# Kernel tuning notes

Measured on AMD Instinct MI355X. Metric: run time of the kernel, lower is better.

The kernel has to match this reference:

```python
import jax, jax.numpy as jnp
import numpy as np

NUM_HEADS = 16
HEIGHT = 32
WIDTH = 32
FEATURES_DIM = HEIGHT * WIDTH  # 1024
EMBED_DIM = 1024


def setup_inputs() -> dict:
    key = jax.random.key(0)
    ks = jax.random.split(key, 9)
    s_in = 1.0 / np.sqrt(FEATURES_DIM)
    s_e = 1.0 / np.sqrt(EMBED_DIM)
    return {
        "x": jax.random.normal(ks[0], (16, 512, HEIGHT, WIDTH), dtype=jnp.float32),
        "Wq": jax.random.uniform(ks[1], (EMBED_DIM, FEATURES_DIM), jnp.float32, -s_in, s_in),
        "bq": jax.random.uniform(ks[2], (EMBED_DIM,), jnp.float32, -s_in, s_in),
        "Wk": jax.random.uniform(ks[3], (EMBED_DIM, FEATURES_DIM), jnp.float32, -s_in, s_in),
        "bk": jax.random.uniform(ks[4], (EMBED_DIM,), jnp.float32, -s_in, s_in),
        "Wv": jax.random.uniform(ks[5], (EMBED_DIM, FEATURES_DIM), jnp.float32, -s_in, s_in),
        "bv": jax.random.uniform(ks[6], (EMBED_DIM,), jnp.float32, -s_in, s_in),
        "Wo": jax.random.uniform(ks[7], (FEATURES_DIM, EMBED_DIM), jnp.float32, -s_e, s_e),
        "bo": jax.random.uniform(ks[8], (FEATURES_DIM,), jnp.float32, -s_e, s_e),
    }


def reference(x, Wq, bq, Wk, bk, Wv, bv, Wo, bo):
    B, C, H, W = x.shape
    nh = NUM_HEADS
    hd = EMBED_DIM // nh
    xf = x.reshape(B, C, H * W)  # [B, C, F] - channel tokens
    q = xf @ Wq.T + bq  # [B, C, E]
    k = xf @ Wk.T + bk
    v = xf @ Wv.T + bv
    q = q.reshape(B, C, nh, hd).transpose(0, 2, 1, 3)  # [B, nh, C, hd]
    k = k.reshape(B, C, nh, hd).transpose(0, 2, 1, 3)
    v = v.reshape(B, C, nh, hd).transpose(0, 2, 1, 3)
    scores = jnp.einsum("bhcd,bhkd->bhck", q, k) / jnp.sqrt(jnp.float32(hd))
    attn = jax.nn.softmax(scores, axis=-1)
    out = jnp.einsum("bhck,bhkd->bhcd", attn, v)  # [B, nh, C, hd]
    out = out.transpose(0, 2, 1, 3).reshape(B, C, EMBED_DIM)
    out = out @ Wo.T + bo  # [B, C, F]
    return out.reshape(B, C, H, W)
```

## Files before the change

### kernel.cpp

```cpp
#include <hip/hip_runtime.h>


typedef unsigned short u16;
typedef __attribute__((ext_vector_type(8))) short short8;
typedef __attribute__((ext_vector_type(4))) float f32x4;
typedef __attribute__((ext_vector_type(4))) unsigned short u16x4;

#define MFMA16(a, b, c) __builtin_amdgcn_mfma_f32_16x16x32_bf16(a, b, c, 0, 0, 0)

__device__ __forceinline__ u16 f2bf(float x) {
  unsigned u = __float_as_uint(x);
  u += 0x7FFFu + ((u >> 16) & 1u);
  return (u16)(u >> 16);
}

__device__ __forceinline__ void async16(const void* g, void* l) {
  __builtin_amdgcn_global_load_lds(
      (__attribute__((address_space(1))) unsigned int*)(g),
      (__attribute__((address_space(3))) unsigned int*)(l), 16, 0, 0);
}

__global__ __launch_bounds__(256) void cvt_all(
    const float* __restrict__ x, const float* __restrict__ wq,
    const float* __restrict__ wk, const float* __restrict__ wv,
    const float* __restrict__ wo, u16* __restrict__ dst) {
  int g = blockIdx.x * 256 + threadIdx.x;
  const float* s;
  int off;
  if (g < 2097152) {
    s = x; off = g;
  } else {
    int r = g - 2097152;
    int w = r >> 18;
    off = r & 262143;
    s = (w == 0) ? wq : (w == 1) ? wk : (w == 2) ? wv : wo;
  }
  f32x4 v = ((const f32x4*)s)[off];
  u16x4 o;
#pragma unroll
  for (int j = 0; j < 4; ++j) o[j] = f2bf(v[j]);
  ((u16x4*)dst)[g] = o;
}

template <int CB, bool ST>
__device__ __forceinline__ void tile256(const u16* lds, const u16* gA,
                                        const u16* gB, u16* stA, u16* stB,
                                        int kn, int arow, int brow, int sw0,
                                        int sw1, short8* a, short8* b,
                                        f32x4 acc[8][4]) {
  constexpr int NB = CB ^ 1;
  const u16* bp = lds + CB * 32768;
#pragma unroll
  for (int mf = 0; mf < 4; ++mf) {
    a[mf * 2 + 0] = *(const short8*)(bp + arow + mf * 1024 + sw0);
    a[mf * 2 + 1] = *(const short8*)(bp + arow + mf * 1024 + sw1);
  }
#pragma unroll
  for (int nf = 0; nf < 2; ++nf) {
    b[nf * 2 + 0] = *(const short8*)(bp + brow + nf * 1024 + sw0);
    b[nf * 2 + 1] = *(const short8*)(bp + brow + nf * 1024 + sw1);
  }
  if (ST) {
    async16(gA + 0 * 65536 + kn, stA + NB * 32768 + 0 * 4096);
    async16(gA + 2 * 65536 + kn, stA + NB * 32768 + 2 * 4096);
    async16(gB + 0 * 65536 + kn, stB + NB * 32768 + 0 * 4096);
    async16(gB + 1 * 65536 + kn, stB + NB * 32768 + 1 * 4096);
  }
  __builtin_amdgcn_s_barrier();
  asm volatile("s_waitcnt lgkmcnt(0)" ::: "memory");
  __builtin_amdgcn_sched_barrier(0);
  __builtin_amdgcn_s_setprio(1);
#pragma unroll
  for (int mf = 0; mf < 4; ++mf)
#pragma unroll
    for (int nf = 0; nf < 2; ++nf) {
      acc[mf][nf] = MFMA16(a[mf * 2 + 0], b[nf * 2 + 0], acc[mf][nf]);
      acc[mf][nf] = MFMA16(a[mf * 2 + 1], b[nf * 2 + 1], acc[mf][nf]);
    }
  __builtin_amdgcn_s_setprio(0);
  __builtin_amdgcn_s_barrier();
#pragma unroll
  for (int nf = 2; nf < 4; ++nf) {
    b[nf * 2 + 0] = *(const short8*)(bp + brow + nf * 1024 + sw0);
    b[nf * 2 + 1] = *(const short8*)(bp + brow + nf * 1024 + sw1);
  }
  if (ST) {
    async16(gB + 2 * 65536 + kn, stB + NB * 32768 + 2 * 4096);
    async16(gB + 3 * 65536 + kn, stB + NB * 32768 + 3 * 4096);
  }
  __builtin_amdgcn_s_barrier();
  asm volatile("s_waitcnt lgkmcnt(0)" ::: "memory");
  __builtin_amdgcn_sched_barrier(0);
  __builtin_amdgcn_s_setprio(1);
#pragma unroll
  for (int mf = 0; mf < 4; ++mf)
#pragma unroll
    for (int nf = 2; nf < 4; ++nf) {
      acc[mf][nf] = MFMA16(a[mf * 2 + 0], b[nf * 2 + 0], acc[mf][nf]);
      acc[mf][nf] = MFMA16(a[mf * 2 + 1], b[nf * 2 + 1], acc[mf][nf]);
    }
  __builtin_amdgcn_s_setprio(0);
  __builtin_amdgcn_s_barrier();
#pragma unroll
  for (int mf = 4; mf < 8; ++mf) {
    a[(mf - 4) * 2 + 0] = *(const short8*)(bp + arow + mf * 1024 + sw0);
    a[(mf - 4) * 2 + 1] = *(const short8*)(bp + arow + mf * 1024 + sw1);
  }
  if (ST) {
    async16(gA + 1 * 65536 + kn, stA + NB * 32768 + 1 * 4096);
    async16(gA + 3 * 65536 + kn, stA + NB * 32768 + 3 * 4096);
  }
  __builtin_amdgcn_s_barrier();
  asm volatile("s_waitcnt lgkmcnt(0)" ::: "memory");
  __builtin_amdgcn_sched_barrier(0);
  __builtin_amdgcn_s_setprio(1);
#pragma unroll
  for (int mf = 4; mf < 8; ++mf)
#pragma unroll
    for (int nf = 2; nf < 4; ++nf) {
      acc[mf][nf] = MFMA16(a[(mf - 4) * 2 + 0], b[nf * 2 + 0], acc[mf][nf]);
      acc[mf][nf] = MFMA16(a[(mf - 4) * 2 + 1], b[nf * 2 + 1], acc[mf][nf]);
    }
  __builtin_amdgcn_s_setprio(0);
  __builtin_amdgcn_s_barrier();
  __builtin_amdgcn_s_setprio(1);
#pragma unroll
  for (int mf = 4; mf < 8; ++mf)
#pragma unroll
    for (int nf = 0; nf < 2; ++nf) {
      acc[mf][nf] = MFMA16(a[(mf - 4) * 2 + 0], b[nf * 2 + 0], acc[mf][nf]);
      acc[mf][nf] = MFMA16(a[(mf - 4) * 2 + 1], b[nf * 2 + 1], acc[mf][nf]);
    }
  __builtin_amdgcn_s_setprio(0);
  asm volatile("s_waitcnt vmcnt(0)" ::: "memory");
  __builtin_amdgcn_s_barrier();
}

__device__ __forceinline__ void gemm256(const u16* __restrict__ A,
                                        const u16* __restrict__ W, int m0,
                                        int n0, u16* lds, f32x4 acc[8][4]) {
  const int t = threadIdx.x;
  const int wave = t >> 6, lane = t & 63, lr = lane & 15, lg = lane >> 4;
  const int wr = wave >> 2, wn = wave & 3;
  const int srow = t >> 3;
  const int scol = ((t & 7) ^ (srow & 7)) << 3;
  const u16* gA = A + (size_t)(m0 + srow) * 1024 + scol;
  const u16* gB = W + (size_t)(n0 + srow) * 1024 + scol;
  u16* stA = lds + wave * 512;
  u16* stB = lds + 16384 + wave * 512;
  const int arow = (wr * 128 + lr) * 64;
  const int brow = 16384 + (wn * 64 + lr) * 64;
  const int xk = lr & 7;
  const int sw0 = (lg ^ xk) << 3;
  const int sw1 = ((4 + lg) ^ xk) << 3;

#pragma unroll
  for (int j = 0; j < 4; ++j) {
    async16(gA + j * 65536, stA + j * 4096);
    async16(gB + j * 65536, stB + j * 4096);
  }
  asm volatile("s_waitcnt vmcnt(0)" ::: "memory");
  __builtin_amdgcn_s_barrier();

  short8 a[8], b[8];
#pragma unroll 1
  for (int it = 0; it < 7; ++it) {
    const int kt = it * 2;
    tile256<0, true>(lds, gA, gB, stA, stB, (kt + 1) * 64, arow, brow, sw0,
                     sw1, a, b, acc);
    tile256<1, true>(lds, gA, gB, stA, stB, (kt + 2) * 64, arow, brow, sw0,
                     sw1, a, b, acc);
  }
  tile256<0, true>(lds, gA, gB, stA, stB, 15 * 64, arow, brow, sw0, sw1, a, b,
                   acc);
  tile256<1, false>(lds, gA, gB, stA, stB, 0, arow, brow, sw0, sw1, a, b, acc);
}

__global__ __launch_bounds__(512, 2) void gemm_qkv(
    const u16* __restrict__ xb, const u16* __restrict__ w3,
    const float* __restrict__ bq, const float* __restrict__ bk,
    const float* __restrict__ bv, u16* __restrict__ qo, u16* __restrict__ ko,
    u16* __restrict__ vo) {
  __shared__ u16 lds[65536];
  const int id = blockIdx.x;
  const int lid = (id & 7) * 48 + (id >> 3);
  const int tm = lid / 12, tn = lid % 12;
  const int m0 = tm * 256, n0g = tn * 256;
  const int z = n0g >> 10, n0 = n0g & 1023;
  const float* bias = (z == 0) ? bq : (z == 1) ? bk : bv;
  u16* outp = (z == 0) ? qo : (z == 1) ? ko : vo;
  f32x4 acc[8][4];
#pragma unroll
  for (int i = 0; i < 8; ++i)
#pragma unroll
    for (int j = 0; j < 4; ++j) acc[i][j] = (f32x4){0.f, 0.f, 0.f, 0.f};
  gemm256(xb, w3, m0, n0g, lds, acc);

  const int t = threadIdx.x;
  const int wave = t >> 6, lane = t & 63, lr = lane & 15, lg = lane >> 4;
  const int wr = wave >> 2, wn = wave & 3;
  float bb[4];
#pragma unroll
  for (int nf = 0; nf < 4; ++nf) bb[nf] = bias[n0 + wn * 64 + nf * 16 + lr];
#pragma unroll
  for (int mf = 0; mf < 8; ++mf)
#pragma unroll
    for (int nf = 0; nf < 4; ++nf)
#pragma unroll
      for (int r = 0; r < 4; ++r) {
        int m = m0 + wr * 128 + mf * 16 + lg * 4 + r;
        int n = n0 + wn * 64 + nf * 16 + lr;
        float val = acc[mf][nf][r] + bb[nf];
        int b_ = m >> 9, c = m & 511, h = n >> 6, dd = n & 63;
        int idx = (z == 2) ? ((((b_ << 4) + h) << 15) + (dd << 9) + c)
                           : ((((b_ << 4) + h) << 15) + (c << 6) + dd);
        outp[idx] = f2bf(val);
      }
}

__global__ __launch_bounds__(512, 2) void gemm_oproj(const u16* __restrict__ ab,
                                                     const u16* __restrict__ wo,
                                                     const float* __restrict__ bo,
                                                     float* __restrict__ out) {
  __shared__ u16 lds[65536];
  const int id = blockIdx.x;
  const int lid = (id & 7) * 16 + (id >> 3);
  const int m0 = (lid >> 2) * 256, n0 = (lid & 3) * 256;
  f32x4 acc[8][4];
#pragma unroll
  for (int i = 0; i < 8; ++i)
#pragma unroll
    for (int j = 0; j < 4; ++j) acc[i][j] = (f32x4){0.f, 0.f, 0.f, 0.f};
  gemm256(ab, wo, m0, n0, lds, acc);

  const int t = threadIdx.x;
  const int wave = t >> 6, lane = t & 63, lr = lane & 15, lg = lane >> 4;
  const int wr = wave >> 2, wn = wave & 3;
  float bb[4];
#pragma unroll
  for (int nf = 0; nf < 4; ++nf) bb[nf] = bo[n0 + wn * 64 + nf * 16 + lr];
#pragma unroll
  for (int mf = 0; mf < 8; ++mf)
#pragma unroll
    for (int nf = 0; nf < 4; ++nf)
#pragma unroll
      for (int r = 0; r < 4; ++r) {
        int m = m0 + wr * 128 + mf * 16 + lg * 4 + r;
        int n = n0 + wn * 64 + nf * 16 + lr;
        out[m * 1024 + n] = acc[mf][nf][r] + bb[nf];
      }
}

__global__ __launch_bounds__(512, 2) void attn_kernel(
    const u16* __restrict__ qb, const u16* __restrict__ kb,
    const u16* __restrict__ vb, u16* __restrict__ ab) {
  __shared__ u16 lK[32768];
  __shared__ u16 lV[32768];
  __shared__ u16 lP[8192];
  const int t = threadIdx.x;
  const int bh = blockIdx.x;
  const int b_ = bh >> 4, h_ = bh & 15;
  const u16* kg = kb + bh * 32768;
  const u16* vg = vb + bh * 32768;
#pragma unroll
  for (int i = 0; i < 8; ++i) {
    int row = i * 64 + (t >> 3), slot = t & 7;
    short8 kv = *(const short8*)(kg + row * 64 + slot * 8);
    *(short8*)(lK + row * 64 + ((slot ^ (row & 7)) << 3)) = kv;
    int vrow = i * 8 + (t >> 6), vslot = t & 63;
    short8 vv = *(const short8*)(vg + vrow * 512 + vslot * 8);
    *(short8*)(lV + vrow * 512 + ((vslot ^ (vrow & 7)) << 3)) = vv;
  }
  __syncthreads();

  const int wv_ = t >> 6, lane = t & 63, lr = lane & 15, lg = lane >> 4;
  u16* lPw = lP + wv_ * 1024;
  const u16* qg = qb + bh * 32768;
  const float sc = 0.125f * 1.44269504088896f;

#pragma unroll 1
  for (int qi = 0; qi < 4; ++qi) {
    const int qrow = (wv_ * 4 + qi) * 16;
    short8 a0 = *(const short8*)(qg + (qrow + lr) * 64 + lg * 8);
    short8 a1 = *(const short8*)(qg + (qrow + lr) * 64 + 32 + lg * 8);
    f32x4 s[32];
#pragma unroll
    for (int f = 0; f < 32; ++f) {
      const u16* kr = lK + (f * 16 + lr) * 64;
      short8 k0 = *(const short8*)(kr + ((lg ^ (lr & 7)) << 3));
      short8 k1 = *(const short8*)(kr + (((4 + lg) ^ (lr & 7)) << 3));
      f32x4 z4 = (f32x4){0.f, 0.f, 0.f, 0.f};
      z4 = MFMA16(a0, k0, z4);
      z4 = MFMA16(a1, k1, z4);
      s[f] = z4;
    }
    float inv[4];
#pragma unroll
    for (int r = 0; r < 4; ++r) {
      float m_ = s[0][r];
#pragma unroll
      for (int f = 1; f < 32; ++f) m_ = fmaxf(m_, s[f][r]);
      m_ = fmaxf(m_, __shfl_xor(m_, 1));
      m_ = fmaxf(m_, __shfl_xor(m_, 2));
      m_ = fmaxf(m_, __shfl_xor(m_, 4));
      m_ = fmaxf(m_, __shfl_xor(m_, 8));
      float sm = 0.f;
#pragma unroll
      for (int f = 0; f < 32; ++f) {
        float e = exp2f((s[f][r] - m_) * sc);
        s[f][r] = e;
        sm += e;
      }
      sm += __shfl_xor(sm, 1);
      sm += __shfl_xor(sm, 2);
      sm += __shfl_xor(sm, 4);
      sm += __shfl_xor(sm, 8);
      inv[r] = 1.f / sm;
    }
    f32x4 o[4];
#pragma unroll
    for (int i = 0; i < 4; ++i) o[i] = (f32x4){0.f, 0.f, 0.f, 0.f};
#pragma unroll
    for (int ch = 0; ch < 8; ++ch) {
#pragma unroll
      for (int cf = 0; cf < 4; ++cf)
#pragma unroll
        for (int r = 0; r < 4; ++r) {
          int q = lg * 4 + r, kc = cf * 16 + lr;
          lPw[q * 64 + (((kc >> 3) ^ (q & 7)) << 3) + (kc & 7)] =
              f2bf(s[ch * 4 + cf][r]);
        }
      asm volatile("s_waitcnt lgkmcnt(0)" ::: "memory");
      const u16* pr = lPw + lr * 64;
      short8 pa0 = *(const short8*)(pr + ((lg ^ (lr & 7)) << 3));
      short8 pa1 = *(const short8*)(pr + (((4 + lg) ^ (lr & 7)) << 3));
#pragma unroll
      for (int df = 0; df < 4; ++df) {
        const u16* vr = lV + (df * 16 + lr) * 512;
        short8 v0 = *(const short8*)(vr + (((ch * 8 + lg) ^ (lr & 7)) << 3));
        short8 v1 =
            *(const short8*)(vr + (((ch * 8 + 4 + lg) ^ (lr & 7)) << 3));
        o[df] = MFMA16(pa0, v0, o[df]);
        o[df] = MFMA16(pa1, v1, o[df]);
      }
    }
#pragma unroll
    for (int df = 0; df < 4; ++df)
#pragma unroll
      for (int r = 0; r < 4; ++r) {
        int q = qrow + lg * 4 + r, dd = df * 16 + lr;
        ab[(b_ * 512 + q) * 1024 + h_ * 64 + dd] = f2bf(o[df][r] * inv[r]);
      }
  }
}

extern "C" void kernel_launch(void* const* d_in, const int* in_sizes, int n_in,
                              void* d_out, int out_size, void* d_ws,
                              size_t ws_size, hipStream_t stream) {
  (void)in_sizes; (void)n_in; (void)out_size;
  const float* x  = (const float*)d_in[0];
  const float* Wq = (const float*)d_in[1];
  const float* bq = (const float*)d_in[2];
  const float* Wk = (const float*)d_in[3];
  const float* bk = (const float*)d_in[4];
  const float* Wv = (const float*)d_in[5];
  const float* bv = (const float*)d_in[6];
  const float* Wo = (const float*)d_in[7];
  const float* bo = (const float*)d_in[8];
  float* out = (float*)d_out;

  if (ws_size < 75497472u) return;
  u16* xb  = (u16*)d_ws;
  u16* w3b = xb + 8388608;
  u16* wob = w3b + 3145728;
  u16* qbuf = wob + 1048576;
  u16* kbuf = qbuf + 8388608;
  u16* vbuf = kbuf + 8388608;
  u16* abuf = xb;

  cvt_all<<<12288, 256, 0, stream>>>(x, Wq, Wk, Wv, Wo, xb);
  gemm_qkv<<<384, 512, 0, stream>>>(xb, w3b, bq, bk, bv, qbuf, kbuf, vbuf);
  attn_kernel<<<256, 512, 0, stream>>>(qbuf, kbuf, vbuf, abuf);
  gemm_oproj<<<128, 512, 0, stream>>>(abuf, wob, bo, out);
}
```

Measured before the change: 173.4 us.

## Deepen GEMM global-to-LDS prefetch pipeline and prefetch Q in attention

Restructures the GEMM main loop so each K tile's global-to-LDS async loads are split into halves issued one and two tiles ahead. Waits use a partial vmcnt instead of draining every outstanding load each tile. This is meant to hide more global memory latency behind MFMA work, at the cost of more LDS buffer hazards to get right. The attention kernel also loads all Q fragments into registers before the K/V staging barrier and raises wave priority around its MFMA blocks.

```diff
diff --git a/kernel.cpp b/kernel.cpp
--- a/kernel.cpp
+++ b/kernel.cpp
@@ -42,103 +42,9 @@
   ((u16x4*)dst)[g] = o;
 }
 
-template <int CB, bool ST>
-__device__ __forceinline__ void tile256(const u16* lds, const u16* gA,
-                                        const u16* gB, u16* stA, u16* stB,
-                                        int kn, int arow, int brow, int sw0,
-                                        int sw1, short8* a, short8* b,
-                                        f32x4 acc[8][4]) {
-  constexpr int NB = CB ^ 1;
-  const u16* bp = lds + CB * 32768;
-#pragma unroll
-  for (int mf = 0; mf < 4; ++mf) {
-    a[mf * 2 + 0] = *(const short8*)(bp + arow + mf * 1024 + sw0);
-    a[mf * 2 + 1] = *(const short8*)(bp + arow + mf * 1024 + sw1);
-  }
-#pragma unroll
-  for (int nf = 0; nf < 2; ++nf) {
-    b[nf * 2 + 0] = *(const short8*)(bp + brow + nf * 1024 + sw0);
-    b[nf * 2 + 1] = *(const short8*)(bp + brow + nf * 1024 + sw1);
-  }
-  if (ST) {
-    async16(gA + 0 * 65536 + kn, stA + NB * 32768 + 0 * 4096);
-    async16(gA + 2 * 65536 + kn, stA + NB * 32768 + 2 * 4096);
-    async16(gB + 0 * 65536 + kn, stB + NB * 32768 + 0 * 4096);
-    async16(gB + 1 * 65536 + kn, stB + NB * 32768 + 1 * 4096);
-  }
-  __builtin_amdgcn_s_barrier();
-  asm volatile("s_waitcnt lgkmcnt(0)" ::: "memory");
-  __builtin_amdgcn_sched_barrier(0);
-  __builtin_amdgcn_s_setprio(1);
-#pragma unroll
-  for (int mf = 0; mf < 4; ++mf)
-#pragma unroll
-    for (int nf = 0; nf < 2; ++nf) {
-      acc[mf][nf] = MFMA16(a[mf * 2 + 0], b[nf * 2 + 0], acc[mf][nf]);
-      acc[mf][nf] = MFMA16(a[mf * 2 + 1], b[nf * 2 + 1], acc[mf][nf]);
-    }
-  __builtin_amdgcn_s_setprio(0);
-  __builtin_amdgcn_s_barrier();
-#pragma unroll
-  for (int nf = 2; nf < 4; ++nf) {
-    b[nf * 2 + 0] = *(const short8*)(bp + brow + nf * 1024 + sw0);
-    b[nf * 2 + 1] = *(const short8*)(bp + brow + nf * 1024 + sw1);
-  }
-  if (ST) {
-    async16(gB + 2 * 65536 + kn, stB + NB * 32768 + 2 * 4096);
-    async16(gB + 3 * 65536 + kn, stB + NB * 32768 + 3 * 4096);
-  }
-  __builtin_amdgcn_s_barrier();
-  asm volatile("s_waitcnt lgkmcnt(0)" ::: "memory");
-  __builtin_amdgcn_sched_barrier(0);
-  __builtin_amdgcn_s_setprio(1);
-#pragma unroll
-  for (int mf = 0; mf < 4; ++mf)
-#pragma unroll
-    for (int nf = 2; nf < 4; ++nf) {
-      acc[mf][nf] = MFMA16(a[mf * 2 + 0], b[nf * 2 + 0], acc[mf][nf]);
-      acc[mf][nf] = MFMA16(a[mf * 2 + 1], b[nf * 2 + 1], acc[mf][nf]);
-    }
-  __builtin_amdgcn_s_setprio(0);
-  __builtin_amdgcn_s_barrier();
-#pragma unroll
-  for (int mf = 4; mf < 8; ++mf) {
-    a[(mf - 4) * 2 + 0] = *(const short8*)(bp + arow + mf * 1024 + sw0);
-    a[(mf - 4) * 2 + 1] = *(const short8*)(bp + arow + mf * 1024 + sw1);
-  }
-  if (ST) {
-    async16(gA + 1 * 65536 + kn, stA + NB * 32768 + 1 * 4096);
-    async16(gA + 3 * 65536 + kn, stA + NB * 32768 + 3 * 4096);
-  }
-  __builtin_amdgcn_s_barrier();
-  asm volatile("s_waitcnt lgkmcnt(0)" ::: "memory");
-  __builtin_amdgcn_sched_barrier(0);
-  __builtin_amdgcn_s_setprio(1);
-#pragma unroll
-  for (int mf = 4; mf < 8; ++mf)
-#pragma unroll
-    for (int nf = 2; nf < 4; ++nf) {
-      acc[mf][nf] = MFMA16(a[(mf - 4) * 2 + 0], b[nf * 2 + 0], acc[mf][nf]);
-      acc[mf][nf] = MFMA16(a[(mf - 4) * 2 + 1], b[nf * 2 + 1], acc[mf][nf]);
-    }
-  __builtin_amdgcn_s_setprio(0);
-  __builtin_amdgcn_s_barrier();
-  __builtin_amdgcn_s_setprio(1);
-#pragma unroll
-  for (int mf = 4; mf < 8; ++mf)
-#pragma unroll
-    for (int nf = 0; nf < 2; ++nf) {
-      acc[mf][nf] = MFMA16(a[(mf - 4) * 2 + 0], b[nf * 2 + 0], acc[mf][nf]);
-      acc[mf][nf] = MFMA16(a[(mf - 4) * 2 + 1], b[nf * 2 + 1], acc[mf][nf]);
-    }
-  __builtin_amdgcn_s_setprio(0);
-  asm volatile("s_waitcnt vmcnt(0)" ::: "memory");
-  __builtin_amdgcn_s_barrier();
-}
-
-__device__ __forceinline__ void gemm256(const u16* __restrict__ A,
-                                        const u16* __restrict__ W, int m0,
-                                        int n0, u16* lds, f32x4 acc[8][4]) {
+__device__ __forceinline__ void gemm8p(const u16* __restrict__ A,
+                                       const u16* __restrict__ W, int m0,
+                                       int n0, u16* lds, f32x4 acc[8][4]) {
   const int t = threadIdx.x;
   const int wave = t >> 6, lane = t & 63, lr = lane & 15, lg = lane >> 4;
   const int wr = wave >> 2, wn = wave & 3;
@@ -154,26 +60,111 @@
   const int sw0 = (lg ^ xk) << 3;
   const int sw1 = ((4 + lg) ^ xk) << 3;
 
-#pragma unroll
-  for (int j = 0; j < 4; ++j) {
-    async16(gA + j * 65536, stA + j * 4096);
-    async16(gB + j * 65536, stB + j * 4096);
-  }
-  asm volatile("s_waitcnt vmcnt(0)" ::: "memory");
+#define SA(kt, h)                                                           \
+  {                                                                         \
+    async16(gA + (2 * (h)) * 65536 + (kt) * 64,                             \
+            stA + ((kt) & 1) * 32768 + (2 * (h)) * 4096);                   \
+    async16(gA + (2 * (h) + 1) * 65536 + (kt) * 64,                         \
+            stA + ((kt) & 1) * 32768 + (2 * (h) + 1) * 4096);               \
+  }
+#define SB(kt, h)                                                           \
+  {                                                                         \
+    async16(gB + (2 * (h)) * 65536 + (kt) * 64,                             \
+            stB + ((kt) & 1) * 32768 + (2 * (h)) * 4096);                   \
+    async16(gB + (2 * (h) + 1) * 65536 + (kt) * 64,                         \
+            stB + ((kt) & 1) * 32768 + (2 * (h) + 1) * 4096);               \
+  }
+
+  SB(0, 0); SA(0, 0); SB(0, 1); SA(0, 1);
+  SB(1, 0); SA(1, 0);
+  asm volatile("s_waitcnt vmcnt(4)" ::: "memory");
   __builtin_amdgcn_s_barrier();
 
   short8 a[8], b[8];
-#pragma unroll 1
-  for (int it = 0; it < 7; ++it) {
-    const int kt = it * 2;
-    tile256<0, true>(lds, gA, gB, stA, stB, (kt + 1) * 64, arow, brow, sw0,
-                     sw1, a, b, acc);
-    tile256<1, true>(lds, gA, gB, stA, stB, (kt + 2) * 64, arow, brow, sw0,
-                     sw1, a, b, acc);
-  }
-  tile256<0, true>(lds, gA, gB, stA, stB, 15 * 64, arow, brow, sw0, sw1, a, b,
-                   acc);
-  tile256<1, false>(lds, gA, gB, stA, stB, 0, arow, brow, sw0, sw1, a, b, acc);
+#pragma unroll 2
+  for (int tt = 0; tt < 16; ++tt) {
+    const u16* bp = lds + (tt & 1) * 32768;
+#pragma unroll
+    for (int mf = 0; mf < 4; ++mf) {
+      a[mf * 2 + 0] = *(const short8*)(bp + arow + mf * 1024 + sw0);
+      a[mf * 2 + 1] = *(const short8*)(bp + arow + mf * 1024 + sw1);
+    }
+#pragma unroll
+    for (int nf = 0; nf < 2; ++nf) {
+      b[nf * 2 + 0] = *(const short8*)(bp + brow + nf * 1024 + sw0);
+      b[nf * 2 + 1] = *(const short8*)(bp + brow + nf * 1024 + sw1);
+    }
+    if (tt + 1 < 16) SB(tt + 1, 1);
+    __builtin_amdgcn_s_barrier();
+    asm volatile("s_waitcnt lgkmcnt(0)" ::: "memory");
+    __builtin_amdgcn_sched_barrier(0);
+    __builtin_amdgcn_s_setprio(1);
+#pragma unroll
+    for (int mf = 0; mf < 4; ++mf)
+#pragma unroll
+      for (int nf = 0; nf < 2; ++nf) {
+        acc[mf][nf] = MFMA16(a[mf * 2 + 0], b[nf * 2 + 0], acc[mf][nf]);
+        acc[mf][nf] = MFMA16(a[mf * 2 + 1], b[nf * 2 + 1], acc[mf][nf]);
+      }
+    __builtin_amdgcn_s_setprio(0);
+    __builtin_amdgcn_s_barrier();
+#pragma unroll
+    for (int nf = 2; nf < 4; ++nf) {
+      b[nf * 2 + 0] = *(const short8*)(bp + brow + nf * 1024 + sw0);
+      b[nf * 2 + 1] = *(const short8*)(bp + brow + nf * 1024 + sw1);
+    }
+    if (tt + 1 < 16) SA(tt + 1, 1);
+    __builtin_amdgcn_s_barrier();
+    asm volatile("s_waitcnt lgkmcnt(0)" ::: "memory");
+    __builtin_amdgcn_sched_barrier(0);
+    __builtin_amdgcn_s_setprio(1);
+#pragma unroll
+    for (int mf = 0; mf < 4; ++mf)
+#pragma unroll
+      for (int nf = 2; nf < 4; ++nf) {
+        acc[mf][nf] = MFMA16(a[mf * 2 + 0], b[nf * 2 + 0], acc[mf][nf]);
+        acc[mf][nf] = MFMA16(a[mf * 2 + 1], b[nf * 2 + 1], acc[mf][nf]);
+      }
+    __builtin_amdgcn_s_setprio(0);
+    __builtin_amdgcn_s_barrier();
+#pragma unroll
+    for (int mf = 4; mf < 8; ++mf) {
+      a[(mf - 4) * 2 + 0] = *(const short8*)(bp + arow + mf * 1024 + sw0);
+      a[(mf - 4) * 2 + 1] = *(const short8*)(bp + arow + mf * 1024 + sw1);
+    }
+    if (tt + 2 < 16) SB(tt + 2, 0);
+    __builtin_amdgcn_s_barrier();
+    asm volatile("s_waitcnt lgkmcnt(0)" ::: "memory");
+    __builtin_amdgcn_sched_barrier(0);
+    __builtin_amdgcn_s_setprio(1);
+#pragma unroll
+    for (int mf = 4; mf < 8; ++mf)
+#pragma unroll
+      for (int nf = 2; nf < 4; ++nf) {
+        acc[mf][nf] = MFMA16(a[(mf - 4) * 2 + 0], b[nf * 2 + 0], acc[mf][nf]);
+        acc[mf][nf] = MFMA16(a[(mf - 4) * 2 + 1], b[nf * 2 + 1], acc[mf][nf]);
+      }
+    __builtin_amdgcn_s_setprio(0);
+    __builtin_amdgcn_s_barrier();
+    if (tt + 2 < 16) SA(tt + 2, 0);
+    __builtin_amdgcn_s_setprio(1);
+#pragma unroll
+    for (int mf = 4; mf < 8; ++mf)
+#pragma unroll
+      for (int nf = 0; nf < 2; ++nf) {
+        acc[mf][nf] = MFMA16(a[(mf - 4) * 2 + 0], b[nf * 2 + 0], acc[mf][nf]);
+        acc[mf][nf] = MFMA16(a[(mf - 4) * 2 + 1], b[nf * 2 + 1], acc[mf][nf]);
+      }
+    __builtin_amdgcn_s_setprio(0);
+    if (tt < 14) {
+      asm volatile("s_waitcnt vmcnt(4)" ::: "memory");
+    } else {
+      asm volatile("s_waitcnt vmcnt(0)" ::: "memory");
+    }
+    __builtin_amdgcn_s_barrier();
+  }
+#undef SA
+#undef SB
 }
 
 __global__ __launch_bounds__(512, 2) void gemm_qkv(
@@ -194,7 +185,7 @@
   for (int i = 0; i < 8; ++i)
 #pragma unroll
     for (int j = 0; j < 4; ++j) acc[i][j] = (f32x4){0.f, 0.f, 0.f, 0.f};
-  gemm256(xb, w3, m0, n0g, lds, acc);
+  gemm8p(xb, w3, m0, n0g, lds, acc);
 
   const int t = threadIdx.x;
   const int wave = t >> 6, lane = t & 63, lr = lane & 15, lg = lane >> 4;
@@ -231,7 +222,7 @@
   for (int i = 0; i < 8; ++i)
 #pragma unroll
     for (int j = 0; j < 4; ++j) acc[i][j] = (f32x4){0.f, 0.f, 0.f, 0.f};
-  gemm256(ab, wo, m0, n0, lds, acc);
+  gemm8p(ab, wo, m0, n0, lds, acc);
 
   const int t = threadIdx.x;
   const int wave = t >> 6, lane = t & 63, lr = lane & 15, lg = lane >> 4;
@@ -271,29 +262,37 @@
     short8 vv = *(const short8*)(vg + vrow * 512 + vslot * 8);
     *(short8*)(lV + vrow * 512 + ((vslot ^ (vrow & 7)) << 3)) = vv;
   }
-  __syncthreads();
 
   const int wv_ = t >> 6, lane = t & 63, lr = lane & 15, lg = lane >> 4;
   u16* lPw = lP + wv_ * 1024;
   const u16* qg = qb + bh * 32768;
   const float sc = 0.125f * 1.44269504088896f;
 
+  short8 a0q[4], a1q[4];
+#pragma unroll
+  for (int qi = 0; qi < 4; ++qi) {
+    const int qrow = (wv_ * 4 + qi) * 16;
+    a0q[qi] = *(const short8*)(qg + (qrow + lr) * 64 + lg * 8);
+    a1q[qi] = *(const short8*)(qg + (qrow + lr) * 64 + 32 + lg * 8);
+  }
+  __syncthreads();
+
 #pragma unroll 1
   for (int qi = 0; qi < 4; ++qi) {
     const int qrow = (wv_ * 4 + qi) * 16;
-    short8 a0 = *(const short8*)(qg + (qrow + lr) * 64 + lg * 8);
-    short8 a1 = *(const short8*)(qg + (qrow + lr) * 64 + 32 + lg * 8);
     f32x4 s[32];
+    __builtin_amdgcn_s_setprio(1);
 #pragma unroll
     for (int f = 0; f < 32; ++f) {
       const u16* kr = lK + (f * 16 + lr) * 64;
       short8 k0 = *(const short8*)(kr + ((lg ^ (lr & 7)) << 3));
       short8 k1 = *(const short8*)(kr + (((4 + lg) ^ (lr & 7)) << 3));
       f32x4 z4 = (f32x4){0.f, 0.f, 0.f, 0.f};
-      z4 = MFMA16(a0, k0, z4);
-      z4 = MFMA16(a1, k1, z4);
+      z4 = MFMA16(a0q[qi], k0, z4);
+      z4 = MFMA16(a1q[qi], k1, z4);
       s[f] = z4;
     }
+    __builtin_amdgcn_s_setprio(0);
     float inv[4];
 #pragma unroll
     for (int r = 0; r < 4; ++r) {
@@ -334,6 +333,7 @@
       const u16* pr = lPw + lr * 64;
       short8 pa0 = *(const short8*)(pr + ((lg ^ (lr & 7)) << 3));
       short8 pa1 = *(const short8*)(pr + (((4 + lg) ^ (lr & 7)) << 3));
+      __builtin_amdgcn_s_setprio(1);
 #pragma unroll
       for (int df = 0; df < 4; ++df) {
         const u16* vr = lV + (df * 16 + lr) * 512;
@@ -343,6 +343,7 @@
         o[df] = MFMA16(pa0, v0, o[df]);
         o[df] = MFMA16(pa1, v1, o[df]);
       }
+      __builtin_amdgcn_s_setprio(0);
     }
 #pragma unroll
     for (int df = 0; df < 4; ++df)
```

After: 186.3 us. +7.4%, slower.
